# Performance work log

Hardware: AMD Instinct MI355X
Metric: run time of the kernel (lower is better)

## Reference

```python
import jax, jax.numpy as jnp
import numpy as np

D_EQUI, D_INV, D_MSG, N_HEADS, D_FF = 64, 256, 64, 8, 256
D_EDGE_IN, D_EDGE_OUT = 64, 64
D_OUT = D_EQUI + N_HEADS + D_EDGE_OUT  # 136
IN_FEATS = 2 * D_MSG + D_EQUI + D_EDGE_IN  # 256
B, N = 4, 256
NEG_INF = -1e9  # finite stand-in for -inf in adj_to_attn_mask


def setup_inputs() -> dict:
    key = jax.random.key(0)
    ks = jax.random.split(key, 20)
    def rn(k, shape, scale):
        return jax.random.normal(k, shape, dtype=jnp.float32) * scale
    inp = {
        "equis": rn(ks[0], (B, N, 3, D_EQUI), 1.0),
        "invs": rn(ks[1], (B, N, D_INV), 1.0),
        "edges": rn(ks[2], (B, N, N, D_EDGE_IN), 1.0),
        "adj_matrix": jax.random.randint(ks[3], (B, N, N), 0, 2, dtype=jnp.int32),
        # _PairwiseMessages params
        "Wq": rn(ks[4], (D_MSG, D_INV), D_INV ** -0.5),
        "bq": jnp.zeros((D_MSG,), jnp.float32),
        "Wk": rn(ks[5], (D_MSG, D_INV), D_INV ** -0.5),
        "bk": jnp.zeros((D_MSG,), jnp.float32),
        "W1": rn(ks[6], (D_FF, IN_FEATS), IN_FEATS ** -0.5),
        "b1": jnp.zeros((D_FF,), jnp.float32),
        "W2": rn(ks[7], (D_OUT, D_FF), D_FF ** -0.5),
        "b2": jnp.zeros((D_OUT,), jnp.float32),
        # _EquiAttention params (no bias)
        "Wc": rn(ks[8], (D_EQUI, D_EQUI), D_EQUI ** -0.5),
        "Wa": rn(ks[9], (D_EQUI, D_EQUI), D_EQUI ** -0.5),
        # _InvAttention params
        "Wi": rn(ks[10], (D_INV, D_INV), D_INV ** -0.5),
        "bi": jnp.zeros((D_INV,), jnp.float32),
        "Wo": rn(ks[11], (D_INV, D_INV), D_INV ** -0.5),
        "bo": jnp.zeros((D_INV,), jnp.float32),
    }
    return inp


def _forward(equis, invs, edges, adj_matrix, Wq, bq, Wk, bk, W1, b1, W2, b2, Wc, Wa, Wi, bi, Wo, bo):
    # ---- _PairwiseMessages ----
    # per-channel dot products over the 3 coordinates: [B, Nq, Nk, d_equi]
    dotprods = jnp.einsum("bqcd,bkcd->bqkd", equis, equis)
    q_msg = invs @ Wq.T + bq          # [B, N, d_msg]
    k_msg = invs @ Wk.T + bk          # [B, N, d_msg]
    Nq = invs.shape[1]
    pairwise = jnp.concatenate(
        (
            jnp.broadcast_to(q_msg[:, :, None, :], (B, Nq, Nq, D_MSG)),
            jnp.broadcast_to(k_msg[:, None, :, :], (B, Nq, Nq, D_MSG)),
            dotprods,
            edges,
        ),
        axis=-1,
    )  # [B, Nq, Nk, in_feats]
    h = jax.nn.silu(pairwise @ W1.T + b1)
    messages = h @ W2.T + b2          # [B, Nq, Nk, d_out]

    equi_msg = messages[..., :D_EQUI]
    inv_msg = messages[..., D_EQUI : D_EQUI + N_HEADS]
    edge_out = messages[..., D_EQUI + N_HEADS :]

    attn_mask = jnp.where(adj_matrix > 0, 0.0, NEG_INF).astype(equi_msg.dtype)  # [B,Nq,Nk]

    # ---- _EquiAttention ----
    attn_e = jax.nn.softmax(equi_msg + attn_mask[..., None], axis=2)  # [B,Nq,Nk,d_equi]
    proj_equi = equis @ Wc.T                                          # [B,Nk,3,d_equi]
    attn_out_e = jnp.einsum("bqkd,bkcd->bqcd", attn_e, proj_equi)     # [B,Nq,3,d_equi]
    w_e = jnp.sqrt(jnp.sum(attn_e ** 2, axis=2))                      # [B,Nq,d_equi]
    attn_out_e = attn_out_e * w_e[:, :, None, :]
    equi_updates = attn_out_e @ Wa.T

    # ---- _InvAttention ----
    attn_i = jax.nn.softmax(inv_msg + attn_mask[..., None], axis=2)   # [B,Nq,Nk,H]
    proj_feats = invs @ Wi.T + bi                                     # [B,Nk,d_inv]
    head_feats = proj_feats.reshape(B, Nq, N_HEADS, D_INV // N_HEADS)
    attn_out_i = jnp.einsum("bqkh,bkhd->bqhd", attn_i, head_feats)    # [B,Nq,H,d_head]
    w_i = jnp.sqrt(jnp.sum(attn_i ** 2, axis=2))                      # [B,Nq,H]
    attn_out_i = attn_out_i * w_i[..., None]
    inv_updates = attn_out_i.reshape(B, Nq, D_INV) @ Wo.T + bo

    return equi_updates, inv_updates, edge_out


def reference(equis, invs, edges, adj_matrix, Wq, bq, Wk, bk, W1, b1, W2, b2, Wc, Wa, Wi, bi, Wo, bo):
    return _forward(equis, invs, edges, adj_matrix, Wq, bq, Wk, bk, W1, b1, W2, b2, Wc, Wa, Wi, bi, Wo, bo)
```

## Files before the change

kernel.cpp:

```cpp
#include <hip/hip_runtime.h>
#include <hip/hip_bf16.h>
#include <cstdint>


typedef __bf16 bf16x8_t __attribute__((ext_vector_type(8)));
typedef float  f32x4_t  __attribute__((ext_vector_type(4)));

#define SP 76
#define KV 32

__device__ __forceinline__ int swzX(int row, int col) {
    return row * 192 + (col ^ ((row & 7) << 3));
}
__device__ __forceinline__ int swzH(int row, int col) {
    return (row << 8) + (col ^ ((row & 7) << 3));
}

__device__ __forceinline__ bf16x8_t cvt8(f32x4_t a, f32x4_t b) {
    bf16x8_t r;
    r[0] = (__bf16)a.x; r[1] = (__bf16)a.y; r[2] = (__bf16)a.z; r[3] = (__bf16)a.w;
    r[4] = (__bf16)b.x; r[5] = (__bf16)b.y; r[6] = (__bf16)b.z; r[7] = (__bf16)b.w;
    return r;
}

__global__ __launch_bounds__(256) void semla_pre(
    const float* __restrict__ invs, const float* __restrict__ equis,
    const float* __restrict__ Wq, const float* __restrict__ bq,
    const float* __restrict__ Wk, const float* __restrict__ bk,
    const float* __restrict__ Wc, const float* __restrict__ Wi, const float* __restrict__ bi,
    const float* __restrict__ W1, const float* __restrict__ W2,
    __bf16* __restrict__ W1bf, __bf16* __restrict__ W2bf,
    float* __restrict__ qc, float* __restrict__ kmsg,
    float* __restrict__ pTE, float* __restrict__ pTF)
{
    const int blk = blockIdx.x, tid = threadIdx.x;
    if (blk < 256) {
        const int r0 = blk * 4;
        __shared__ __align__(16) float sInv4[4][256];
        __shared__ __align__(16) float sEqu4[4][192];
        __shared__ __align__(16) float sQm4[4][64];
        #pragma unroll
        for (int j = 0; j < 4; ++j) {
            sInv4[j][tid] = invs[(size_t)(r0 + j) * 256 + tid];
            if (tid < 192) sEqu4[j][tid] = equis[(size_t)(r0 + j) * 192 + tid];
        }
        __syncthreads();
        {
            float acc[4] = {0.f, 0.f, 0.f, 0.f};
            const float* w = &Wi[tid * 256];
            for (int i = 0; i < 256; i += 4) {
                f32x4_t ww = *(const f32x4_t*)&w[i];
                #pragma unroll
                for (int j = 0; j < 4; ++j) {
                    const float* x = &sInv4[j][i];
                    acc[j] += ww.x * x[0] + ww.y * x[1] + ww.z * x[2] + ww.w * x[3];
                }
            }
            const float bb = bi[tid];
            #pragma unroll
            for (int j = 0; j < 4; ++j) {
                const int bb_ = (r0 + j) >> 8, nl = (r0 + j) & 255;
                pTF[((size_t)bb_ * 256 + tid) * 256 + nl] = acc[j] + bb;
            }
        }
        if (tid < 128) {
            const int d = tid & 63;
            const float* w = (tid < 64) ? &Wq[d * 256] : &Wk[d * 256];
            float acc[4] = {0.f, 0.f, 0.f, 0.f};
            for (int i = 0; i < 256; i += 4) {
                f32x4_t ww = *(const f32x4_t*)&w[i];
                #pragma unroll
                for (int j = 0; j < 4; ++j) {
                    const float* x = &sInv4[j][i];
                    acc[j] += ww.x * x[0] + ww.y * x[1] + ww.z * x[2] + ww.w * x[3];
                }
            }
            if (tid < 64) {
                const float bb = bq[d];
                #pragma unroll
                for (int j = 0; j < 4; ++j) sQm4[j][d] = acc[j] + bb;
            } else {
                const float bb = bk[d];
                #pragma unroll
                for (int j = 0; j < 4; ++j) kmsg[(size_t)(r0 + j) * 64 + d] = acc[j] + bb;
            }
        }
        if (tid < 192) {
            const int c = tid >> 6, e = tid & 63;
            const float* w = &Wc[e * 64];
            float acc[4] = {0.f, 0.f, 0.f, 0.f};
            for (int dd = 0; dd < 64; dd += 4) {
                f32x4_t ww = *(const f32x4_t*)&w[dd];
                #pragma unroll
                for (int j = 0; j < 4; ++j) {
                    const float* x = &sEqu4[j][c * 64 + dd];
                    acc[j] += ww.x * x[0] + ww.y * x[1] + ww.z * x[2] + ww.w * x[3];
                }
            }
            #pragma unroll
            for (int j = 0; j < 4; ++j) {
                const int bb_ = (r0 + j) >> 8, nl = (r0 + j) & 255;
                pTE[(((size_t)bb_ * 3 + c) * 64 + e) * 256 + nl] = acc[j];
            }
        }
        __syncthreads();
        {
            const float* w = &W1[tid * 256];
            float acc[4] = {0.f, 0.f, 0.f, 0.f};
            for (int d = 0; d < 64; d += 4) {
                f32x4_t ww = *(const f32x4_t*)&w[d];
                #pragma unroll
                for (int j = 0; j < 4; ++j) {
                    const float* x = &sQm4[j][d];
                    acc[j] += ww.x * x[0] + ww.y * x[1] + ww.z * x[2] + ww.w * x[3];
                }
            }
            #pragma unroll
            for (int j = 0; j < 4; ++j) qc[(size_t)(r0 + j) * 256 + tid] = acc[j];
        }
    } else if (blk < 268) {
        const int base = (blk - 256) * 4096;
        #pragma unroll
        for (int it = 0; it < 16; ++it) {
            const int e = base + it * 256 + tid;
            const int o = e / 192, k = e % 192;
            W1bf[e] = (__bf16)W1[o * 256 + 64 + k];
        }
    } else if (blk < 277) {
        const int base = (blk - 268) * 4096;
        #pragma unroll
        for (int it = 0; it < 16; ++it) {
            const int e = base + it * 256 + tid;
            const int o = e >> 8, cc = e & 255;
            const int src = (o < 64) ? (72 + o) : (o < 136 ? o - 64 : -1);
            W2bf[e] = (src >= 0) ? (__bf16)W2[src * 256 + cc] : (__bf16)0.f;
        }
    }
}

__global__ __launch_bounds__(512, 2) void semla_main(
    const float* __restrict__ equis, const float* __restrict__ edges,
    const int* __restrict__ adj,
    const __bf16* __restrict__ W1bf, const __bf16* __restrict__ W2bf,
    const float* __restrict__ qc, const float* __restrict__ kmsg,
    const float* __restrict__ pTE, const float* __restrict__ pTF,
    const float* __restrict__ b1, const float* __restrict__ b2,
    float* __restrict__ outE, float* __restrict__ outI, float* __restrict__ outEdge)
{
    const int bqid = ((blockIdx.x & 7) << 7) | (blockIdx.x >> 3);
    const int b = bqid >> 8;
    const int tid = threadIdx.x;
    const int wave = tid >> 6, lane = tid & 63;
    const int arow = lane & 15, kgrp = lane >> 4;

    __shared__ __align__(16) __bf16 sX[KV * 192];
    __shared__ __align__(16) __bf16 sH[KV * 256];
    __shared__ __align__(16) float  sS[KV * SP];
    __shared__ __align__(16) float  sB1[256];
    __shared__ __align__(16) float  sB2[144];
    __shared__ __align__(16) float  sEquiQ[192];
    __shared__ float sF[72], sL[72], sL2[72];
    __shared__ int   sAdj[KV];

    if (tid < 256) sB1[tid] = b1[tid] + qc[(size_t)bqid * 256 + tid];
    if (tid < 144) sB2[tid] = (tid < 64) ? b2[72 + tid] : (tid < 136 ? b2[tid - 64] : 0.f);
    if (tid < 192) sEquiQ[tid] = equis[(size_t)bqid * 192 + tid];

    bf16x8_t w1r[6][2];
    #pragma unroll
    for (int ks = 0; ks < 6; ++ks)
        #pragma unroll
        for (int cf = 0; cf < 2; ++cf)
            w1r[ks][cf] = *(const bf16x8_t*)
                &W1bf[((wave << 5) + (cf << 4) + arow) * 192 + ks * 32 + (kgrp << 3)];
    bf16x8_t w2r[8], w2r2[8];
    #pragma unroll
    for (int ks = 0; ks < 8; ++ks)
        w2r[ks] = *(const bf16x8_t*)
            &W2bf[(((wave << 4) + arow) << 8) + ks * 32 + (kgrp << 3)];
    if (wave == 7) {
        #pragma unroll
        for (int ks = 0; ks < 8; ++ks)
            w2r2[ks] = *(const bf16x8_t*)
                &W2bf[((128 + arow) << 8) + ks * 32 + (kgrp << 3)];
    }

    float m_run = -1e30f, l_run = 0.f, l2_run = 0.f;
    float m_rn2 = -1e30f, l_rn2 = 0.f, l2_rn2 = 0.f;
    float accE = 0.f;
    float accI = 0.f;
    const int c_e = tid >> 6, d_e = tid & 63;
    const int fidx = tid - 256, h_i = (tid - 256) >> 5;

    __syncthreads();

    for (int kt = 0; kt < 8; ++kt) {
        const int k0 = kt * KV;
        const int kb = b * 256 + k0;

        #pragma unroll
        for (int gi = 0; gi < 2; ++gi) {
            const int g = (gi == 0) ? tid : 512 + tid;
            if (gi == 1 && tid >= 256) continue;
            const int row = g / 24, c8 = (g % 24) << 3;
            if (c8 < 64) {
                const float* p = &kmsg[(size_t)(kb + row) * 64 + c8];
                *(bf16x8_t*)&sX[swzX(row, c8)] =
                    cvt8(*(const f32x4_t*)p, *(const f32x4_t*)(p + 4));
            } else if (c8 < 128) {
                const int d0 = c8 - 64;
                const float* ek = &equis[(size_t)(kb + row) * 192 + d0];
                f32x4_t e0a = *(const f32x4_t*)(ek),       e0b = *(const f32x4_t*)(ek + 4);
                f32x4_t e1a = *(const f32x4_t*)(ek + 64),  e1b = *(const f32x4_t*)(ek + 68);
                f32x4_t e2a = *(const f32x4_t*)(ek + 128), e2b = *(const f32x4_t*)(ek + 132);
                f32x4_t q0a = *(const f32x4_t*)&sEquiQ[d0],       q0b = *(const f32x4_t*)&sEquiQ[d0 + 4];
                f32x4_t q1a = *(const f32x4_t*)&sEquiQ[64 + d0],  q1b = *(const f32x4_t*)&sEquiQ[68 + d0];
                f32x4_t q2a = *(const f32x4_t*)&sEquiQ[128 + d0], q2b = *(const f32x4_t*)&sEquiQ[132 + d0];
                *(bf16x8_t*)&sX[swzX(row, c8)] =
                    cvt8(e0a * q0a + e1a * q1a + e2a * q2a,
                         e0b * q0b + e1b * q1b + e2b * q2b);
            } else {
                const float* p = &edges[((size_t)bqid * 256 + k0 + row) * 64 + (c8 - 128)];
                *(bf16x8_t*)&sX[swzX(row, c8)] =
                    cvt8(*(const f32x4_t*)p, *(const f32x4_t*)(p + 4));
            }
        }
        if (tid < KV) sAdj[tid] = adj[(size_t)bqid * 256 + k0 + tid];
        if (kt > 0) {
            const int k0P = k0 - KV;
            if (tid < 192) {
                float a = accE * sF[d_e];
                const float* pe = &pTE[(((size_t)b * 3 + c_e) * 64 + d_e) * 256 + k0P];
                #pragma unroll
                for (int t = 0; t < 8; ++t) {
                    f32x4_t w = *(const f32x4_t*)&pe[t * 4];
                    a += sS[(4 * t + 0) * SP + d_e] * w.x;
                    a += sS[(4 * t + 1) * SP + d_e] * w.y;
                    a += sS[(4 * t + 2) * SP + d_e] * w.z;
                    a += sS[(4 * t + 3) * SP + d_e] * w.w;
                }
                accE = a;
            }
            if (tid >= 256) {
                float a = accI * sF[64 + h_i];
                const float* pf = &pTF[((size_t)b * 256 + fidx) * 256 + k0P];
                #pragma unroll
                for (int t = 0; t < 8; ++t) {
                    f32x4_t w = *(const f32x4_t*)&pf[t * 4];
                    a += sS[(4 * t + 0) * SP + 64 + h_i] * w.x;
                    a += sS[(4 * t + 1) * SP + 64 + h_i] * w.y;
                    a += sS[(4 * t + 2) * SP + 64 + h_i] * w.z;
                    a += sS[(4 * t + 3) * SP + 64 + h_i] * w.w;
                }
                accI = a;
            }
        }
        __syncthreads();

        f32x4_t acc1[2][2];
        {
            const f32x4_t z = {0.f, 0.f, 0.f, 0.f};
            acc1[0][0] = z; acc1[0][1] = z; acc1[1][0] = z; acc1[1][1] = z;
        }
        #pragma unroll
        for (int ks = 0; ks < 6; ++ks) {
            const int kk = ks * 32 + (kgrp << 3);
            bf16x8_t a0 = *(const bf16x8_t*)&sX[swzX(arow, kk)];
            bf16x8_t a1 = *(const bf16x8_t*)&sX[swzX(16 + arow, kk)];
            acc1[0][0] = __builtin_amdgcn_mfma_f32_16x16x32_bf16(a0, w1r[ks][0], acc1[0][0], 0, 0, 0);
            acc1[0][1] = __builtin_amdgcn_mfma_f32_16x16x32_bf16(a0, w1r[ks][1], acc1[0][1], 0, 0, 0);
            acc1[1][0] = __builtin_amdgcn_mfma_f32_16x16x32_bf16(a1, w1r[ks][0], acc1[1][0], 0, 0, 0);
            acc1[1][1] = __builtin_amdgcn_mfma_f32_16x16x32_bf16(a1, w1r[ks][1], acc1[1][1], 0, 0, 0);
        }
        #pragma unroll
        for (int rt = 0; rt < 2; ++rt)
            #pragma unroll
            for (int cf = 0; cf < 2; ++cf) {
                const int ccol = (wave << 5) + (cf << 4) + arow;
                const float bb = sB1[ccol];
                #pragma unroll
                for (int j = 0; j < 4; ++j) {
                    const int row = (rt << 4) + (kgrp << 2) + j;
                    float x = acc1[rt][cf][j] + bb;
                    sH[swzH(row, ccol)] = (__bf16)(x / (1.f + __expf(-x)));
                }
            }
        __syncthreads();

        f32x4_t acc2[2], acc2b[2];
        {
            const f32x4_t z = {0.f, 0.f, 0.f, 0.f};
            acc2[0] = z; acc2[1] = z; acc2b[0] = z; acc2b[1] = z;
        }
        #pragma unroll
        for (int ks = 0; ks < 8; ++ks) {
            const int kk = ks * 32 + (kgrp << 3);
            bf16x8_t a0 = *(const bf16x8_t*)&sH[swzH(arow, kk)];
            bf16x8_t a1 = *(const bf16x8_t*)&sH[swzH(16 + arow, kk)];
            acc2[0] = __builtin_amdgcn_mfma_f32_16x16x32_bf16(a0, w2r[ks], acc2[0], 0, 0, 0);
            acc2[1] = __builtin_amdgcn_mfma_f32_16x16x32_bf16(a1, w2r[ks], acc2[1], 0, 0, 0);
            if (wave == 7) {
                acc2b[0] = __builtin_amdgcn_mfma_f32_16x16x32_bf16(a0, w2r2[ks], acc2b[0], 0, 0, 0);
                acc2b[1] = __builtin_amdgcn_mfma_f32_16x16x32_bf16(a1, w2r2[ks], acc2b[1], 0, 0, 0);
            }
        }
        const int col = (wave << 4) + arow;
        if (wave < 4) {
            const float bb2 = sB2[col];
            #pragma unroll
            for (int rt = 0; rt < 2; ++rt)
                #pragma unroll
                for (int j = 0; j < 4; ++j) {
                    const int r = (rt << 4) + (kgrp << 2) + j;
                    outEdge[((size_t)bqid * 256 + k0 + r) * 64 + col] = acc2[rt][j] + bb2;
                }
        } else {
            const int ch = col - 64;
            const float bb2 = sB2[col];
            float s_[8]; int ad_[8];
            float xm = -1e30f;
            #pragma unroll
            for (int rt = 0; rt < 2; ++rt)
                #pragma unroll
                for (int j = 0; j < 4; ++j) {
                    const int r = (rt << 4) + (kgrp << 2) + j;
                    const float v = acc2[rt][j] + bb2;
                    s_[rt * 4 + j] = v;
                    ad_[rt * 4 + j] = sAdj[r];
                    if (ad_[rt * 4 + j]) xm = fmaxf(xm, v);
                }
            xm = fmaxf(xm, __shfl_xor(xm, 16));
            xm = fmaxf(xm, __shfl_xor(xm, 32));
            const float mN = fmaxf(m_run, xm);
            const float f = __expf(m_run - mN);
            float s1 = 0.f, s2 = 0.f;
            #pragma unroll
            for (int rt = 0; rt < 2; ++rt)
                #pragma unroll
                for (int j = 0; j < 4; ++j) {
                    const int r = (rt << 4) + (kgrp << 2) + j;
                    const float p = ad_[rt * 4 + j] ? __expf(s_[rt * 4 + j] - mN) : 0.f;
                    sS[r * SP + ch] = p;
                    s1 += p; s2 += p * p;
                }
            s1 += __shfl_xor(s1, 16); s1 += __shfl_xor(s1, 32);
            s2 += __shfl_xor(s2, 16); s2 += __shfl_xor(s2, 32);
            l_run = l_run * f + s1;
            l2_run = l2_run * f * f + s2;
            m_run = mN;
            if (kgrp == 0) sF[ch] = f;
        }
        if (wave == 7) {
            const float bb3 = sB2[128 + (arow & 7)];
            float s_[8]; int ad_[8];
            float xm = -1e30f;
            #pragma unroll
            for (int rt = 0; rt < 2; ++rt)
                #pragma unroll
                for (int j = 0; j < 4; ++j) {
                    const int r = (rt << 4) + (kgrp << 2) + j;
                    const float v = acc2b[rt][j] + bb3;
                    s_[rt * 4 + j] = v;
                    ad_[rt * 4 + j] = sAdj[r];
                    if (ad_[rt * 4 + j]) xm = fmaxf(xm, v);
                }
            xm = fmaxf(xm, __shfl_xor(xm, 16));
            xm = fmaxf(xm, __shfl_xor(xm, 32));
            const float mN = fmaxf(m_rn2, xm);
            const float f = __expf(m_rn2 - mN);
            float s1 = 0.f, s2 = 0.f;
            #pragma unroll
            for (int rt = 0; rt < 2; ++rt)
                #pragma unroll
                for (int j = 0; j < 4; ++j) {
                    const int r = (rt << 4) + (kgrp << 2) + j;
                    const float p = ad_[rt * 4 + j] ? __expf(s_[rt * 4 + j] - mN) : 0.f;
                    if (arow < 8) sS[r * SP + 64 + arow] = p;
                    s1 += p; s2 += p * p;
                }
            s1 += __shfl_xor(s1, 16); s1 += __shfl_xor(s1, 32);
            s2 += __shfl_xor(s2, 16); s2 += __shfl_xor(s2, 32);
            l_rn2 = l_rn2 * f + s1;
            l2_rn2 = l2_rn2 * f * f + s2;
            m_rn2 = mN;
            if (kgrp == 0 && arow < 8) sF[64 + arow] = f;
        }
        __syncthreads();
    }

    {
        const int k0P = 224;
        if (tid < 192) {
            float a = accE * sF[d_e];
            const float* pe = &pTE[(((size_t)b * 3 + c_e) * 64 + d_e) * 256 + k0P];
            #pragma unroll
            for (int t = 0; t < 8; ++t) {
                f32x4_t w = *(const f32x4_t*)&pe[t * 4];
                a += sS[(4 * t + 0) * SP + d_e] * w.x;
                a += sS[(4 * t + 1) * SP + d_e] * w.y;
                a += sS[(4 * t + 2) * SP + d_e] * w.z;
                a += sS[(4 * t + 3) * SP + d_e] * w.w;
            }
            accE = a;
        }
        if (tid >= 256) {
            float a = accI * sF[64 + h_i];
            const float* pf = &pTF[((size_t)b * 256 + fidx) * 256 + k0P];
            #pragma unroll
            for (int t = 0; t < 8; ++t) {
                f32x4_t w = *(const f32x4_t*)&pf[t * 4];
                a += sS[(4 * t + 0) * SP + 64 + h_i] * w.x;
                a += sS[(4 * t + 1) * SP + 64 + h_i] * w.y;
                a += sS[(4 * t + 2) * SP + 64 + h_i] * w.z;
                a += sS[(4 * t + 3) * SP + 64 + h_i] * w.w;
            }
            accI = a;
        }
    }

    if (wave >= 4 && kgrp == 0) {
        const int ch = ((wave - 4) << 4) + arow;
        sL[ch] = l_run; sL2[ch] = l2_run;
        if (wave == 7 && arow < 8) { sL[64 + arow] = l_rn2; sL2[64 + arow] = l2_rn2; }
    }
    __syncthreads();
    if (tid < 192) {
        const float ll = sL[d_e];
        outE[(size_t)bqid * 192 + tid] = accE * sqrtf(sL2[d_e]) / (ll * ll);
    }
    if (tid >= 256) {
        const float ll = sL[64 + h_i];
        outI[(size_t)bqid * 256 + fidx] = accI * sqrtf(sL2[64 + h_i]) / (ll * ll);
    }
}

__global__ __launch_bounds__(256) void semla_post(
    const float* __restrict__ Wa, const float* __restrict__ Wo,
    const float* __restrict__ bo,
    float* __restrict__ outE, float* __restrict__ outI)
{
    __shared__ __align__(16) float hE[4][192];
    __shared__ __align__(16) float hI[4][256];
    const int blk = blockIdx.x, tid = threadIdx.x;
    const int r0 = blk * 4;
    #pragma unroll
    for (int r = 0; r < 4; ++r) {
        if (tid < 192) hE[r][tid] = outE[(size_t)(r0 + r) * 192 + tid];
        hI[r][tid] = outI[(size_t)(r0 + r) * 256 + tid];
    }
    __syncthreads();
    if (tid < 192) {
        const int c = tid >> 6, e = tid & 63;
        float wa[64];
        #pragma unroll
        for (int d = 0; d < 64; d += 4) {
            f32x4_t w = *(const f32x4_t*)&Wa[e * 64 + d];
            wa[d] = w.x; wa[d + 1] = w.y; wa[d + 2] = w.z; wa[d + 3] = w.w;
        }
        #pragma unroll
        for (int r = 0; r < 4; ++r) {
            float s = 0.f;
            #pragma unroll
            for (int d = 0; d < 64; ++d) s += hE[r][c * 64 + d] * wa[d];
            outE[((size_t)(r0 + r) * 3 + c) * 64 + e] = s;
        }
    }
    {
        const float bb = bo[tid];
        const float* wo = &Wo[tid * 256];
        #pragma unroll
        for (int r = 0; r < 4; ++r) {
            float s = 0.f;
            for (int i = 0; i < 256; i += 4) {
                f32x4_t w = *(const f32x4_t*)&wo[i];
                s += w.x * hI[r][i] + w.y * hI[r][i + 1]
                   + w.z * hI[r][i + 2] + w.w * hI[r][i + 3];
            }
            outI[(size_t)(r0 + r) * 256 + tid] = s + bb;
        }
    }
}

extern "C" void kernel_launch(void* const* d_in, const int* in_sizes, int n_in,
                              void* d_out, int out_size, void* d_ws, size_t ws_size,
                              hipStream_t stream) {
    (void)in_sizes; (void)n_in; (void)out_size; (void)ws_size;
    const float* equis = (const float*)d_in[0];
    const float* invs  = (const float*)d_in[1];
    const float* edges = (const float*)d_in[2];
    const int*   adj   = (const int*)d_in[3];
    const float* Wq = (const float*)d_in[4];
    const float* bq = (const float*)d_in[5];
    const float* Wk = (const float*)d_in[6];
    const float* bk = (const float*)d_in[7];
    const float* W1 = (const float*)d_in[8];
    const float* b1 = (const float*)d_in[9];
    const float* W2 = (const float*)d_in[10];
    const float* b2 = (const float*)d_in[11];
    const float* Wc = (const float*)d_in[12];
    const float* Wa = (const float*)d_in[13];
    const float* Wi = (const float*)d_in[14];
    const float* bi = (const float*)d_in[15];
    const float* Wo = (const float*)d_in[16];
    const float* bo = (const float*)d_in[17];

    float* out = (float*)d_out;
    float* outE    = out;
    float* outI    = out + 196608;
    float* outEdge = out + 458752;

    char* ws = (char*)d_ws;
    __bf16* W1bf = (__bf16*)(ws);
    __bf16* W2bf = (__bf16*)(ws + 98304);
    float* qc    = (float*)(ws + 172032);
    float* kmsg  = (float*)(ws + 1220608);
    float* pTE   = (float*)(ws + 1482752);
    float* pTF   = (float*)(ws + 2269184);

    semla_pre<<<277, 256, 0, stream>>>(invs, equis, Wq, bq, Wk, bk, Wc, Wi, bi,
                                       W1, W2, W1bf, W2bf, qc, kmsg, pTE, pTF);
    semla_main<<<1024, 512, 0, stream>>>(equis, edges, adj, W1bf, W2bf, qc, kmsg,
                                         pTE, pTF, b1, b2,
                                         outE, outI, outEdge);
    semla_post<<<256, 256, 0, stream>>>(Wa, Wo, bo, outE, outI);
}
```

Before: 299.5 us.

## Process two query rows per block to amortize weight loads and key tiles

Each block of the main kernel now handles two adjacent query rows instead of one, and the grid is halved to 512 blocks. Register-resident W1/W2 fragments, the key-message and equis loads, and the pTE/pTF projection loads are shared across both queries. Shared memory and accumulator state are duplicated per query. This raises LDS use and register pressure, which may lower occupancy, and with 512 blocks there are fewer waves to hide latency.

```diff
diff --git a/kernel.cpp b/kernel.cpp
--- a/kernel.cpp
+++ b/kernel.cpp
@@ -147,24 +147,35 @@
     const float* __restrict__ b1, const float* __restrict__ b2,
     float* __restrict__ outE, float* __restrict__ outI, float* __restrict__ outEdge)
 {
-    const int bqid = ((blockIdx.x & 7) << 7) | (blockIdx.x >> 3);
-    const int b = bqid >> 8;
+    const int pair = ((blockIdx.x & 7) << 6) | (blockIdx.x >> 3);
+    const int b = pair >> 7;
+    const int bq0 = b * 256 + ((pair & 127) << 1);
+    const int bq1 = bq0 + 1;
     const int tid = threadIdx.x;
     const int wave = tid >> 6, lane = tid & 63;
     const int arow = lane & 15, kgrp = lane >> 4;
 
-    __shared__ __align__(16) __bf16 sX[KV * 192];
-    __shared__ __align__(16) __bf16 sH[KV * 256];
-    __shared__ __align__(16) float  sS[KV * SP];
-    __shared__ __align__(16) float  sB1[256];
+    __shared__ __align__(16) __bf16 sX0[KV * 192];
+    __shared__ __align__(16) __bf16 sX1[KV * 192];
+    __shared__ __align__(16) __bf16 sH0[KV * 256];
+    __shared__ __align__(16) __bf16 sH1[KV * 256];
+    __shared__ __align__(16) float  sS0[KV * SP];
+    __shared__ __align__(16) float  sS1[KV * SP];
+    __shared__ __align__(16) float  sB1q0[256], sB1q1[256];
     __shared__ __align__(16) float  sB2[144];
-    __shared__ __align__(16) float  sEquiQ[192];
-    __shared__ float sF[72], sL[72], sL2[72];
-    __shared__ int   sAdj[KV];
-
-    if (tid < 256) sB1[tid] = b1[tid] + qc[(size_t)bqid * 256 + tid];
+    __shared__ __align__(16) float  sEquiQ0[192], sEquiQ1[192];
+    __shared__ float sF0[72], sF1[72], sL0[72], sL20[72], sL1[72], sL21[72];
+    __shared__ int   sAdj0[KV], sAdj1[KV];
+
+    if (tid < 256) {
+        sB1q0[tid] = b1[tid] + qc[(size_t)bq0 * 256 + tid];
+        sB1q1[tid] = b1[tid] + qc[(size_t)bq1 * 256 + tid];
+    }
     if (tid < 144) sB2[tid] = (tid < 64) ? b2[72 + tid] : (tid < 136 ? b2[tid - 64] : 0.f);
-    if (tid < 192) sEquiQ[tid] = equis[(size_t)bqid * 192 + tid];
+    if (tid < 192) {
+        sEquiQ0[tid] = equis[(size_t)bq0 * 192 + tid];
+        sEquiQ1[tid] = equis[(size_t)bq1 * 192 + tid];
+    }
 
     bf16x8_t w1r[6][2];
     #pragma unroll
@@ -185,10 +196,12 @@
                 &W2bf[((128 + arow) << 8) + ks * 32 + (kgrp << 3)];
     }
 
-    float m_run = -1e30f, l_run = 0.f, l2_run = 0.f;
-    float m_rn2 = -1e30f, l_rn2 = 0.f, l2_rn2 = 0.f;
-    float accE = 0.f;
-    float accI = 0.f;
+    float m0 = -1e30f, l0 = 0.f, l20 = 0.f;
+    float m1 = -1e30f, l1 = 0.f, l21 = 0.f;
+    float mb0 = -1e30f, lb0 = 0.f, l2b0 = 0.f;
+    float mb1 = -1e30f, lb1 = 0.f, l2b1 = 0.f;
+    float accE0 = 0.f, accE1 = 0.f;
+    float accI0 = 0.f, accI1 = 0.f;
     const int c_e = tid >> 6, d_e = tid & 63;
     const int fidx = tid - 256, h_i = (tid - 256) >> 5;
 
@@ -205,103 +218,149 @@
             const int row = g / 24, c8 = (g % 24) << 3;
             if (c8 < 64) {
                 const float* p = &kmsg[(size_t)(kb + row) * 64 + c8];
-                *(bf16x8_t*)&sX[swzX(row, c8)] =
-                    cvt8(*(const f32x4_t*)p, *(const f32x4_t*)(p + 4));
+                bf16x8_t v = cvt8(*(const f32x4_t*)p, *(const f32x4_t*)(p + 4));
+                *(bf16x8_t*)&sX0[swzX(row, c8)] = v;
+                *(bf16x8_t*)&sX1[swzX(row, c8)] = v;
             } else if (c8 < 128) {
                 const int d0 = c8 - 64;
                 const float* ek = &equis[(size_t)(kb + row) * 192 + d0];
                 f32x4_t e0a = *(const f32x4_t*)(ek),       e0b = *(const f32x4_t*)(ek + 4);
                 f32x4_t e1a = *(const f32x4_t*)(ek + 64),  e1b = *(const f32x4_t*)(ek + 68);
                 f32x4_t e2a = *(const f32x4_t*)(ek + 128), e2b = *(const f32x4_t*)(ek + 132);
-                f32x4_t q0a = *(const f32x4_t*)&sEquiQ[d0],       q0b = *(const f32x4_t*)&sEquiQ[d0 + 4];
-                f32x4_t q1a = *(const f32x4_t*)&sEquiQ[64 + d0],  q1b = *(const f32x4_t*)&sEquiQ[68 + d0];
-                f32x4_t q2a = *(const f32x4_t*)&sEquiQ[128 + d0], q2b = *(const f32x4_t*)&sEquiQ[132 + d0];
-                *(bf16x8_t*)&sX[swzX(row, c8)] =
-                    cvt8(e0a * q0a + e1a * q1a + e2a * q2a,
-                         e0b * q0b + e1b * q1b + e2b * q2b);
+                {
+                    f32x4_t q0a = *(const f32x4_t*)&sEquiQ0[d0],       q0b = *(const f32x4_t*)&sEquiQ0[d0 + 4];
+                    f32x4_t q1a = *(const f32x4_t*)&sEquiQ0[64 + d0],  q1b = *(const f32x4_t*)&sEquiQ0[68 + d0];
+                    f32x4_t q2a = *(const f32x4_t*)&sEquiQ0[128 + d0], q2b = *(const f32x4_t*)&sEquiQ0[132 + d0];
+                    *(bf16x8_t*)&sX0[swzX(row, c8)] =
+                        cvt8(e0a * q0a + e1a * q1a + e2a * q2a,
+                             e0b * q0b + e1b * q1b + e2b * q2b);
+                }
+                {
+                    f32x4_t q0a = *(const f32x4_t*)&sEquiQ1[d0],       q0b = *(const f32x4_t*)&sEquiQ1[d0 + 4];
+                    f32x4_t q1a = *(const f32x4_t*)&sEquiQ1[64 + d0],  q1b = *(const f32x4_t*)&sEquiQ1[68 + d0];
+                    f32x4_t q2a = *(const f32x4_t*)&sEquiQ1[128 + d0], q2b = *(const f32x4_t*)&sEquiQ1[132 + d0];
+                    *(bf16x8_t*)&sX1[swzX(row, c8)] =
+                        cvt8(e0a * q0a + e1a * q1a + e2a * q2a,
+                             e0b * q0b + e1b * q1b + e2b * q2b);
+                }
             } else {
-                const float* p = &edges[((size_t)bqid * 256 + k0 + row) * 64 + (c8 - 128)];
-                *(bf16x8_t*)&sX[swzX(row, c8)] =
-                    cvt8(*(const f32x4_t*)p, *(const f32x4_t*)(p + 4));
-            }
-        }
-        if (tid < KV) sAdj[tid] = adj[(size_t)bqid * 256 + k0 + tid];
+                const float* p0 = &edges[((size_t)bq0 * 256 + k0 + row) * 64 + (c8 - 128)];
+                const float* p1 = &edges[((size_t)bq1 * 256 + k0 + row) * 64 + (c8 - 128)];
+                *(bf16x8_t*)&sX0[swzX(row, c8)] =
+                    cvt8(*(const f32x4_t*)p0, *(const f32x4_t*)(p0 + 4));
+                *(bf16x8_t*)&sX1[swzX(row, c8)] =
+                    cvt8(*(const f32x4_t*)p1, *(const f32x4_t*)(p1 + 4));
+            }
+        }
+        if (tid < KV) {
+            sAdj0[tid] = adj[(size_t)bq0 * 256 + k0 + tid];
+            sAdj1[tid] = adj[(size_t)bq1 * 256 + k0 + tid];
+        }
         if (kt > 0) {
             const int k0P = k0 - KV;
             if (tid < 192) {
-                float a = accE * sF[d_e];
+                float a0 = accE0 * sF0[d_e];
+                float a1 = accE1 * sF1[d_e];
                 const float* pe = &pTE[(((size_t)b * 3 + c_e) * 64 + d_e) * 256 + k0P];
                 #pragma unroll
                 for (int t = 0; t < 8; ++t) {
                     f32x4_t w = *(const f32x4_t*)&pe[t * 4];
-                    a += sS[(4 * t + 0) * SP + d_e] * w.x;
-                    a += sS[(4 * t + 1) * SP + d_e] * w.y;
-                    a += sS[(4 * t + 2) * SP + d_e] * w.z;
-                    a += sS[(4 * t + 3) * SP + d_e] * w.w;
-                }
-                accE = a;
+                    a0 += sS0[(4 * t + 0) * SP + d_e] * w.x;
+                    a0 += sS0[(4 * t + 1) * SP + d_e] * w.y;
+                    a0 += sS0[(4 * t + 2) * SP + d_e] * w.z;
+                    a0 += sS0[(4 * t + 3) * SP + d_e] * w.w;
+                    a1 += sS1[(4 * t + 0) * SP + d_e] * w.x;
+                    a1 += sS1[(4 * t + 1) * SP + d_e] * w.y;
+                    a1 += sS1[(4 * t + 2) * SP + d_e] * w.z;
+                    a1 += sS1[(4 * t + 3) * SP + d_e] * w.w;
+                }
+                accE0 = a0; accE1 = a1;
             }
             if (tid >= 256) {
-                float a = accI * sF[64 + h_i];
+                float a0 = accI0 * sF0[64 + h_i];
+                float a1 = accI1 * sF1[64 + h_i];
                 const float* pf = &pTF[((size_t)b * 256 + fidx) * 256 + k0P];
                 #pragma unroll
                 for (int t = 0; t < 8; ++t) {
                     f32x4_t w = *(const f32x4_t*)&pf[t * 4];
-                    a += sS[(4 * t + 0) * SP + 64 + h_i] * w.x;
-                    a += sS[(4 * t + 1) * SP + 64 + h_i] * w.y;
-                    a += sS[(4 * t + 2) * SP + 64 + h_i] * w.z;
-                    a += sS[(4 * t + 3) * SP + 64 + h_i] * w.w;
-                }
-                accI = a;
+                    a0 += sS0[(4 * t + 0) * SP + 64 + h_i] * w.x;
+                    a0 += sS0[(4 * t + 1) * SP + 64 + h_i] * w.y;
+                    a0 += sS0[(4 * t + 2) * SP + 64 + h_i] * w.z;
+                    a0 += sS0[(4 * t + 3) * SP + 64 + h_i] * w.w;
+                    a1 += sS1[(4 * t + 0) * SP + 64 + h_i] * w.x;
+                    a1 += sS1[(4 * t + 1) * SP + 64 + h_i] * w.y;
+                    a1 += sS1[(4 * t + 2) * SP + 64 + h_i] * w.z;
+                    a1 += sS1[(4 * t + 3) * SP + 64 + h_i] * w.w;
+                }
+                accI0 = a0; accI1 = a1;
             }
         }
         __syncthreads();
 
-        f32x4_t acc1[2][2];
+        f32x4_t A0[2][2], A1[2][2];
         {
             const f32x4_t z = {0.f, 0.f, 0.f, 0.f};
-            acc1[0][0] = z; acc1[0][1] = z; acc1[1][0] = z; acc1[1][1] = z;
+            #pragma unroll
+            for (int rt = 0; rt < 2; ++rt)
+                #pragma unroll
+                for (int cf = 0; cf < 2; ++cf) { A0[rt][cf] = z; A1[rt][cf] = z; }
         }
         #pragma unroll
         for (int ks = 0; ks < 6; ++ks) {
             const int kk = ks * 32 + (kgrp << 3);
-            bf16x8_t a0 = *(const bf16x8_t*)&sX[swzX(arow, kk)];
-            bf16x8_t a1 = *(const bf16x8_t*)&sX[swzX(16 + arow, kk)];
-            acc1[0][0] = __builtin_amdgcn_mfma_f32_16x16x32_bf16(a0, w1r[ks][0], acc1[0][0], 0, 0, 0);
-            acc1[0][1] = __builtin_amdgcn_mfma_f32_16x16x32_bf16(a0, w1r[ks][1], acc1[0][1], 0, 0, 0);
-            acc1[1][0] = __builtin_amdgcn_mfma_f32_16x16x32_bf16(a1, w1r[ks][0], acc1[1][0], 0, 0, 0);
-            acc1[1][1] = __builtin_amdgcn_mfma_f32_16x16x32_bf16(a1, w1r[ks][1], acc1[1][1], 0, 0, 0);
+            bf16x8_t x00 = *(const bf16x8_t*)&sX0[swzX(arow, kk)];
+            bf16x8_t x01 = *(const bf16x8_t*)&sX0[swzX(16 + arow, kk)];
+            bf16x8_t x10 = *(const bf16x8_t*)&sX1[swzX(arow, kk)];
+            bf16x8_t x11 = *(const bf16x8_t*)&sX1[swzX(16 + arow, kk)];
+            A0[0][0] = __builtin_amdgcn_mfma_f32_16x16x32_bf16(x00, w1r[ks][0], A0[0][0], 0, 0, 0);
+            A0[0][1] = __builtin_amdgcn_mfma_f32_16x16x32_bf16(x00, w1r[ks][1], A0[0][1], 0, 0, 0);
+            A0[1][0] = __builtin_amdgcn_mfma_f32_16x16x32_bf16(x01, w1r[ks][0], A0[1][0], 0, 0, 0);
+            A0[1][1] = __builtin_amdgcn_mfma_f32_16x16x32_bf16(x01, w1r[ks][1], A0[1][1], 0, 0, 0);
+            A1[0][0] = __builtin_amdgcn_mfma_f32_16x16x32_bf16(x10, w1r[ks][0], A1[0][0], 0, 0, 0);
+            A1[0][1] = __builtin_amdgcn_mfma_f32_16x16x32_bf16(x10, w1r[ks][1], A1[0][1], 0, 0, 0);
+            A1[1][0] = __builtin_amdgcn_mfma_f32_16x16x32_bf16(x11, w1r[ks][0], A1[1][0], 0, 0, 0);
+            A1[1][1] = __builtin_amdgcn_mfma_f32_16x16x32_bf16(x11, w1r[ks][1], A1[1][1], 0, 0, 0);
         }
         #pragma unroll
         for (int rt = 0; rt < 2; ++rt)
             #pragma unroll
             for (int cf = 0; cf < 2; ++cf) {
                 const int ccol = (wave << 5) + (cf << 4) + arow;
-                const float bb = sB1[ccol];
+                const float bb0 = sB1q0[ccol];
+                const float bb1 = sB1q1[ccol];
                 #pragma unroll
                 for (int j = 0; j < 4; ++j) {
                     const int row = (rt << 4) + (kgrp << 2) + j;
-                    float x = acc1[rt][cf][j] + bb;
-                    sH[swzH(row, ccol)] = (__bf16)(x / (1.f + __expf(-x)));
+                    float x0 = A0[rt][cf][j] + bb0;
+                    float x1 = A1[rt][cf][j] + bb1;
+                    sH0[swzH(row, ccol)] = (__bf16)(x0 / (1.f + __expf(-x0)));
+                    sH1[swzH(row, ccol)] = (__bf16)(x1 / (1.f + __expf(-x1)));
                 }
             }
         __syncthreads();
 
-        f32x4_t acc2[2], acc2b[2];
+        f32x4_t C0[2], C1[2], Cb0[2], Cb1[2];
         {
             const f32x4_t z = {0.f, 0.f, 0.f, 0.f};
-            acc2[0] = z; acc2[1] = z; acc2b[0] = z; acc2b[1] = z;
+            C0[0] = z; C0[1] = z; C1[0] = z; C1[1] = z;
+            Cb0[0] = z; Cb0[1] = z; Cb1[0] = z; Cb1[1] = z;
         }
         #pragma unroll
         for (int ks = 0; ks < 8; ++ks) {
             const int kk = ks * 32 + (kgrp << 3);
-            bf16x8_t a0 = *(const bf16x8_t*)&sH[swzH(arow, kk)];
-            bf16x8_t a1 = *(const bf16x8_t*)&sH[swzH(16 + arow, kk)];
-            acc2[0] = __builtin_amdgcn_mfma_f32_16x16x32_bf16(a0, w2r[ks], acc2[0], 0, 0, 0);
-            acc2[1] = __builtin_amdgcn_mfma_f32_16x16x32_bf16(a1, w2r[ks], acc2[1], 0, 0, 0);
+            bf16x8_t h00 = *(const bf16x8_t*)&sH0[swzH(arow, kk)];
+            bf16x8_t h01 = *(const bf16x8_t*)&sH0[swzH(16 + arow, kk)];
+            bf16x8_t h10 = *(const bf16x8_t*)&sH1[swzH(arow, kk)];
+            bf16x8_t h11 = *(const bf16x8_t*)&sH1[swzH(16 + arow, kk)];
+            C0[0] = __builtin_amdgcn_mfma_f32_16x16x32_bf16(h00, w2r[ks], C0[0], 0, 0, 0);
+            C0[1] = __builtin_amdgcn_mfma_f32_16x16x32_bf16(h01, w2r[ks], C0[1], 0, 0, 0);
+            C1[0] = __builtin_amdgcn_mfma_f32_16x16x32_bf16(h10, w2r[ks], C1[0], 0, 0, 0);
+            C1[1] = __builtin_amdgcn_mfma_f32_16x16x32_bf16(h11, w2r[ks], C1[1], 0, 0, 0);
             if (wave == 7) {
-                acc2b[0] = __builtin_amdgcn_mfma_f32_16x16x32_bf16(a0, w2r2[ks], acc2b[0], 0, 0, 0);
-                acc2b[1] = __builtin_amdgcn_mfma_f32_16x16x32_bf16(a1, w2r2[ks], acc2b[1], 0, 0, 0);
+                Cb0[0] = __builtin_amdgcn_mfma_f32_16x16x32_bf16(h00, w2r2[ks], Cb0[0], 0, 0, 0);
+                Cb0[1] = __builtin_amdgcn_mfma_f32_16x16x32_bf16(h01, w2r2[ks], Cb0[1], 0, 0, 0);
+                Cb1[0] = __builtin_amdgcn_mfma_f32_16x16x32_bf16(h10, w2r2[ks], Cb1[0], 0, 0, 0);
+                Cb1[1] = __builtin_amdgcn_mfma_f32_16x16x32_bf16(h11, w2r2[ks], Cb1[1], 0, 0, 0);
             }
         }
         const int col = (wave << 4) + arow;
@@ -312,78 +371,151 @@
                 #pragma unroll
                 for (int j = 0; j < 4; ++j) {
                     const int r = (rt << 4) + (kgrp << 2) + j;
-                    outEdge[((size_t)bqid * 256 + k0 + r) * 64 + col] = acc2[rt][j] + bb2;
+                    outEdge[((size_t)bq0 * 256 + k0 + r) * 64 + col] = C0[rt][j] + bb2;
+                    outEdge[((size_t)bq1 * 256 + k0 + r) * 64 + col] = C1[rt][j] + bb2;
                 }
         } else {
             const int ch = col - 64;
             const float bb2 = sB2[col];
-            float s_[8]; int ad_[8];
-            float xm = -1e30f;
-            #pragma unroll
-            for (int rt = 0; rt < 2; ++rt)
-                #pragma unroll
-                for (int j = 0; j < 4; ++j) {
-                    const int r = (rt << 4) + (kgrp << 2) + j;
-                    const float v = acc2[rt][j] + bb2;
-                    s_[rt * 4 + j] = v;
-                    ad_[rt * 4 + j] = sAdj[r];
-                    if (ad_[rt * 4 + j]) xm = fmaxf(xm, v);
-                }
-            xm = fmaxf(xm, __shfl_xor(xm, 16));
-            xm = fmaxf(xm, __shfl_xor(xm, 32));
-            const float mN = fmaxf(m_run, xm);
-            const float f = __expf(m_run - mN);
-            float s1 = 0.f, s2 = 0.f;
-            #pragma unroll
-            for (int rt = 0; rt < 2; ++rt)
-                #pragma unroll
-                for (int j = 0; j < 4; ++j) {
-                    const int r = (rt << 4) + (kgrp << 2) + j;
-                    const float p = ad_[rt * 4 + j] ? __expf(s_[rt * 4 + j] - mN) : 0.f;
-                    sS[r * SP + ch] = p;
-                    s1 += p; s2 += p * p;
-                }
-            s1 += __shfl_xor(s1, 16); s1 += __shfl_xor(s1, 32);
-            s2 += __shfl_xor(s2, 16); s2 += __shfl_xor(s2, 32);
-            l_run = l_run * f + s1;
-            l2_run = l2_run * f * f + s2;
-            m_run = mN;
-            if (kgrp == 0) sF[ch] = f;
+            {
+                float s_[8]; int ad_[8];
+                float xm = -1e30f;
+                #pragma unroll
+                for (int rt = 0; rt < 2; ++rt)
+                    #pragma unroll
+                    for (int j = 0; j < 4; ++j) {
+                        const int r = (rt << 4) + (kgrp << 2) + j;
+                        const float v = C0[rt][j] + bb2;
+                        s_[rt * 4 + j] = v;
+                        ad_[rt * 4 + j] = sAdj0[r];
+                        if (ad_[rt * 4 + j]) xm = fmaxf(xm, v);
+                    }
+                xm = fmaxf(xm, __shfl_xor(xm, 16));
+                xm = fmaxf(xm, __shfl_xor(xm, 32));
+                const float mN = fmaxf(m0, xm);
+                const float f = __expf(m0 - mN);
+                float s1 = 0.f, s2 = 0.f;
+                #pragma unroll
+                for (int rt = 0; rt < 2; ++rt)
+                    #pragma unroll
+                    for (int j = 0; j < 4; ++j) {
+                        const int r = (rt << 4) + (kgrp << 2) + j;
+                        const float p = ad_[rt * 4 + j] ? __expf(s_[rt * 4 + j] - mN) : 0.f;
+                        sS0[r * SP + ch] = p;
+                        s1 += p; s2 += p * p;
+                    }
+                s1 += __shfl_xor(s1, 16); s1 += __shfl_xor(s1, 32);
+                s2 += __shfl_xor(s2, 16); s2 += __shfl_xor(s2, 32);
+                l0 = l0 * f + s1;
+                l20 = l20 * f * f + s2;
+                m0 = mN;
+                if (kgrp == 0) sF0[ch] = f;
+            }
+            {
+                float s_[8]; int ad_[8];
+                float xm = -1e30f;
+                #pragma unroll
+                for (int rt = 0; rt < 2; ++rt)
+                    #pragma unroll
+                    for (int j = 0; j < 4; ++j) {
+                        const int r = (rt << 4) + (kgrp << 2) + j;
+                        const float v = C1[rt][j] + bb2;
+                        s_[rt * 4 + j] = v;
+                        ad_[rt * 4 + j] = sAdj1[r];
+                        if (ad_[rt * 4 + j]) xm = fmaxf(xm, v);
+                    }
+                xm = fmaxf(xm, __shfl_xor(xm, 16));
+                xm = fmaxf(xm, __shfl_xor(xm, 32));
+                const float mN = fmaxf(m1, xm);
+                const float f = __expf(m1 - mN);
+                float s1 = 0.f, s2 = 0.f;
+                #pragma unroll
+                for (int rt = 0; rt < 2; ++rt)
+                    #pragma unroll
+                    for (int j = 0; j < 4; ++j) {
+                        const int r = (rt << 4) + (kgrp << 2) + j;
+                        const float p = ad_[rt * 4 + j] ? __expf(s_[rt * 4 + j] - mN) : 0.f;
+                        sS1[r * SP + ch] = p;
+                        s1 += p; s2 += p * p;
+                    }
+                s1 += __shfl_xor(s1, 16); s1 += __shfl_xor(s1, 32);
+                s2 += __shfl_xor(s2, 16); s2 += __shfl_xor(s2, 32);
+                l1 = l1 * f + s1;
+                l21 = l21 * f * f + s2;
+                m1 = mN;
+                if (kgrp == 0) sF1[ch] = f;
+            }
         }
         if (wave == 7) {
             const float bb3 = sB2[128 + (arow & 7)];
-            float s_[8]; int ad_[8];
-            float xm = -1e30f;
-            #pragma unroll
-            for (int rt = 0; rt < 2; ++rt)
-                #pragma unroll
-                for (int j = 0; j < 4; ++j) {
-                    const int r = (rt << 4) + (kgrp << 2) + j;
-                    const float v = acc2b[rt][j] + bb3;
-                    s_[rt * 4 + j] = v;
-                    ad_[rt * 4 + j] = sAdj[r];
-                    if (ad_[rt * 4 + j]) xm = fmaxf(xm, v);
-                }
-            xm = fmaxf(xm, __shfl_xor(xm, 16));
-            xm = fmaxf(xm, __shfl_xor(xm, 32));
-            const float mN = fmaxf(m_rn2, xm);
-            const float f = __expf(m_rn2 - mN);
-            float s1 = 0.f, s2 = 0.f;
-            #pragma unroll
-            for (int rt = 0; rt < 2; ++rt)
-                #pragma unroll
-                for (int j = 0; j < 4; ++j) {
-                    const int r = (rt << 4) + (kgrp << 2) + j;
-                    const float p = ad_[rt * 4 + j] ? __expf(s_[rt * 4 + j] - mN) : 0.f;
-                    if (arow < 8) sS[r * SP + 64 + arow] = p;
-                    s1 += p; s2 += p * p;
-                }
-            s1 += __shfl_xor(s1, 16); s1 += __shfl_xor(s1, 32);
-            s2 += __shfl_xor(s2, 16); s2 += __shfl_xor(s2, 32);
-            l_rn2 = l_rn2 * f + s1;
-            l2_rn2 = l2_rn2 * f * f + s2;
-            m_rn2 = mN;
-            if (kgrp == 0 && arow < 8) sF[64 + arow] = f;
+            {
+                float s_[8]; int ad_[8];
+                float xm = -1e30f;
+                #pragma unroll
+                for (int rt = 0; rt < 2; ++rt)
+                    #pragma unroll
+                    for (int j = 0; j < 4; ++j) {
+                        const int r = (rt << 4) + (kgrp << 2) + j;
+                        const float v = Cb0[rt][j] + bb3;
+                        s_[rt * 4 + j] = v;
+                        ad_[rt * 4 + j] = sAdj0[r];
+                        if (ad_[rt * 4 + j]) xm = fmaxf(xm, v);
+                    }
+                xm = fmaxf(xm, __shfl_xor(xm, 16));
+                xm = fmaxf(xm, __shfl_xor(xm, 32));
+                const float mN = fmaxf(mb0, xm);
+                const float f = __expf(mb0 - mN);
+                float s1 = 0.f, s2 = 0.f;
+                #pragma unroll
+                for (int rt = 0; rt < 2; ++rt)
+                    #pragma unroll
+                    for (int j = 0; j < 4; ++j) {
+                        const int r = (rt << 4) + (kgrp << 2) + j;
+                        const float p = ad_[rt * 4 + j] ? __expf(s_[rt * 4 + j] - mN) : 0.f;
+                        if (arow < 8) sS0[r * SP + 64 + arow] = p;
+                        s1 += p; s2 += p * p;
+                    }
+                s1 += __shfl_xor(s1, 16); s1 += __shfl_xor(s1, 32);
+                s2 += __shfl_xor(s2, 16); s2 += __shfl_xor(s2, 32);
+                lb0 = lb0 * f + s1;
+                l2b0 = l2b0 * f * f + s2;
+                mb0 = mN;
+                if (kgrp == 0 && arow < 8) sF0[64 + arow] = f;
+            }
+            {
+                float s_[8]; int ad_[8];
+                float xm = -1e30f;
+                #pragma unroll
+                for (int rt = 0; rt < 2; ++rt)
+                    #pragma unroll
+                    for (int j = 0; j < 4; ++j) {
+                        const int r = (rt << 4) + (kgrp << 2) + j;
+                        const float v = Cb1[rt][j] + bb3;
+                        s_[rt * 4 + j] = v;
+                        ad_[rt * 4 + j] = sAdj1[r];
+                        if (ad_[rt * 4 + j]) xm = fmaxf(xm, v);
+                    }
+                xm = fmaxf(xm, __shfl_xor(xm, 16));
+                xm = fmaxf(xm, __shfl_xor(xm, 32));
+                const float mN = fmaxf(mb1, xm);
+                const float f = __expf(mb1 - mN);
+                float s1 = 0.f, s2 = 0.f;
+                #pragma unroll
+                for (int rt = 0; rt < 2; ++rt)
+                    #pragma unroll
+                    for (int j = 0; j < 4; ++j) {
+                        const int r = (rt << 4) + (kgrp << 2) + j;
+                        const float p = ad_[rt * 4 + j] ? __expf(s_[rt * 4 + j] - mN) : 0.f;
+                        if (arow < 8) sS1[r * SP + 64 + arow] = p;
+                        s1 += p; s2 += p * p;
+                    }
+                s1 += __shfl_xor(s1, 16); s1 += __shfl_xor(s1, 32);
+                s2 += __shfl_xor(s2, 16); s2 += __shfl_xor(s2, 32);
+                lb1 = lb1 * f + s1;
+                l2b1 = l2b1 * f * f + s2;
+                mb1 = mN;
+                if (kgrp == 0 && arow < 8) sF1[64 + arow] = f;
+            }
         }
         __syncthreads();
     }
@@ -391,46 +523,62 @@
     {
         const int k0P = 224;
         if (tid < 192) {
-            float a = accE * sF[d_e];
+            float a0 = accE0 * sF0[d_e];
+            float a1 = accE1 * sF1[d_e];
             const float* pe = &pTE[(((size_t)b * 3 + c_e) * 64 + d_e) * 256 + k0P];
             #pragma unroll
             for (int t = 0; t < 8; ++t) {
                 f32x4_t w = *(const f32x4_t*)&pe[t * 4];
-                a += sS[(4 * t + 0) * SP + d_e] * w.x;
-                a += sS[(4 * t + 1) * SP + d_e] * w.y;
-                a += sS[(4 * t + 2) * SP + d_e] * w.z;
-                a += sS[(4 * t + 3) * SP + d_e] * w.w;
-            }
-            accE = a;
+                a0 += sS0[(4 * t + 0) * SP + d_e] * w.x;
+                a0 += sS0[(4 * t + 1) * SP + d_e] * w.y;
+                a0 += sS0[(4 * t + 2) * SP + d_e] * w.z;
+                a0 += sS0[(4 * t + 3) * SP + d_e] * w.w;
+                a1 += sS1[(4 * t + 0) * SP + d_e] * w.x;
+                a1 += sS1[(4 * t + 1) * SP + d_e] * w.y;
+                a1 += sS1[(4 * t + 2) * SP + d_e] * w.z;
+                a1 += sS1[(4 * t + 3) * SP + d_e] * w.w;
+            }
+            accE0 = a0; accE1 = a1;
         }
         if (tid >= 256) {
-            float a = accI * sF[64 + h_i];
+            float a0 = accI0 * sF0[64 + h_i];
+            float a1 = accI1 * sF1[64 + h_i];
             const float* pf = &pTF[((size_t)b * 256 + fidx) * 256 + k0P];
             #pragma unroll
             for (int t = 0; t < 8; ++t) {
                 f32x4_t w = *(const f32x4_t*)&pf[t * 4];
-                a += sS[(4 * t + 0) * SP + 64 + h_i] * w.x;
-                a += sS[(4 * t + 1) * SP + 64 + h_i] * w.y;
-                a += sS[(4 * t + 2) * SP + 64 + h_i] * w.z;
-                a += sS[(4 * t + 3) * SP + 64 + h_i] * w.w;
-            }
-            accI = a;
+                a0 += sS0[(4 * t + 0) * SP + 64 + h_i] * w.x;
+                a0 += sS0[(4 * t + 1) * SP + 64 + h_i] * w.y;
+                a0 += sS0[(4 * t + 2) * SP + 64 + h_i] * w.z;
+                a0 += sS0[(4 * t + 3) * SP + 64 + h_i] * w.w;
+                a1 += sS1[(4 * t + 0) * SP + 64 + h_i] * w.x;
+                a1 += sS1[(4 * t + 1) * SP + 64 + h_i] * w.y;
+                a1 += sS1[(4 * t + 2) * SP + 64 + h_i] * w.z;
+                a1 += sS1[(4 * t + 3) * SP + 64 + h_i] * w.w;
+            }
+            accI0 = a0; accI1 = a1;
         }
     }
 
     if (wave >= 4 && kgrp == 0) {
         const int ch = ((wave - 4) << 4) + arow;
-        sL[ch] = l_run; sL2[ch] = l2_run;
-        if (wave == 7 && arow < 8) { sL[64 + arow] = l_rn2; sL2[64 + arow] = l2_rn2; }
+        sL0[ch] = l0; sL20[ch] = l20;
+        sL1[ch] = l1; sL21[ch] = l21;
+        if (wave == 7 && arow < 8) {
+            sL0[64 + arow] = lb0; sL20[64 + arow] = l2b0;
+            sL1[64 + arow] = lb1; sL21[64 + arow] = l2b1;
+        }
     }
     __syncthreads();
     if (tid < 192) {
-        const float ll = sL[d_e];
-        outE[(size_t)bqid * 192 + tid] = accE * sqrtf(sL2[d_e]) / (ll * ll);
+        const float la = sL0[d_e], lbq = sL1[d_e];
+        outE[(size_t)bq0 * 192 + tid] = accE0 * sqrtf(sL20[d_e]) / (la * la);
+        outE[(size_t)bq1 * 192 + tid] = accE1 * sqrtf(sL21[d_e]) / (lbq * lbq);
     }
     if (tid >= 256) {
-        const float ll = sL[64 + h_i];
-        outI[(size_t)bqid * 256 + fidx] = accI * sqrtf(sL2[64 + h_i]) / (ll * ll);
+        const float la = sL0[64 + h_i], lbq = sL1[64 + h_i];
+        outI[(size_t)bq0 * 256 + fidx] = accI0 * sqrtf(sL20[64 + h_i]) / (la * la);
+        outI[(size_t)bq1 * 256 + fidx] = accI1 * sqrtf(sL21[64 + h_i]) / (lbq * lbq);
     }
 }
 
@@ -519,8 +667,8 @@
 
     semla_pre<<<277, 256, 0, stream>>>(invs, equis, Wq, bq, Wk, bk, Wc, Wi, bi,
                                        W1, W2, W1bf, W2bf, qc, kmsg, pTE, pTF);
-    semla_main<<<1024, 512, 0, stream>>>(equis, edges, adj, W1bf, W2bf, qc, kmsg,
-                                         pTE, pTF, b1, b2,
-                                         outE, outI, outEdge);
+    semla_main<<<512, 512, 0, stream>>>(equis, edges, adj, W1bf, W2bf, qc, kmsg,
+                                        pTE, pTF, b1, b2,
+                                        outE, outI, outEdge);
     semla_post<<<256, 256, 0, stream>>>(Wa, Wo, bo, outE, outI);
 }
```

Measured after the change: 373.6 us. +24.7%, slower.
